# Kernel optimization log

Hardware: AMD Instinct MI355X
Metric: run time of the kernel (lower is better)

Reference implementation:

```python
import jax, jax.numpy as jnp
import numpy as np

B, E, T, N = 1024, 512, 8, 256


def setup_inputs() -> dict:
    key = jax.random.key(0)
    k1, k2, k3, k4 = jax.random.split(key, 4)
    weights = jax.random.uniform(k1, (T,), dtype=jnp.float32)  # one scalar per bond type
    bond_src = jax.random.randint(k2, (B, E), 0, N - 1, dtype=jnp.int32)  # raw i, offset +1 later
    bond_dst = jax.random.randint(k3, (B, E), 0, N - 1, dtype=jnp.int32)
    bond_type = jax.random.randint(k4, (B, E), 0, T, dtype=jnp.int32)
    return {"weights": weights, "bond_src": bond_src, "bond_dst": bond_dst,
            "bond_type": bond_type, "num_nodes": N}


def reference(weights, bond_src, bond_dst, bond_type, num_nodes):
    # Gather per-bond weight, then symmetric scatter into dense [B, N, N] adjacency.
    batch, n_edges = bond_src.shape
    w = weights[bond_type]                                  # [B, E] gather
    bidx = jnp.broadcast_to(jnp.arange(batch)[:, None], (batch, n_edges))
    src = bond_src + 1                                      # +1 node offset as in torch code
    dst = bond_dst + 1
    bond_matrix = jnp.zeros((batch, num_nodes, num_nodes), dtype=weights.dtype)
    bond_matrix = bond_matrix.at[bidx, src, dst].set(w)
    bond_matrix = bond_matrix.at[bidx, dst, src].set(w)
    return bond_matrix
```

## Files before the change

kernel.cpp:

```cpp
#include <hip/hip_runtime.h>


#define NB_E 512
#define NB_N 256
#define CH_ROWS 64
#define CH_WORDS (CH_ROWS * NB_N / 2)

typedef float v4f __attribute__((ext_vector_type(4)));

__device__ __forceinline__ void lds_max_u16(unsigned int* tab, int cell, unsigned int v16)
{
    unsigned int* w = tab + (cell >> 1);
    const int sh = (cell & 1) * 16;
    unsigned int old = *w;
    while (true) {
        const unsigned int cur = (old >> sh) & 0xFFFFu;
        if (cur >= v16) break;
        const unsigned int nw = (old & ~(0xFFFFu << sh)) | (v16 << sh);
        const unsigned int seen = atomicCAS(w, old, nw);
        if (seen == old) break;
        old = seen;
    }
}

__global__ __launch_bounds__(256) void BondWeight_41738492182540_kernel(
    const float* __restrict__ weights,
    const int*   __restrict__ bsrc,
    const int*   __restrict__ bdst,
    const int*   __restrict__ btyp,
    float*       __restrict__ out)
{
    __shared__ unsigned int seqtab[CH_WORDS];
    __shared__ float s_wt[8];

    const int b = blockIdx.x;
    const int t = threadIdx.x;

    if (t < 8) s_wt[t] = weights[t];

    const int ebase = b * NB_E;
    int row[4], col[4];
    unsigned int pk[4];
    #pragma unroll
    for (int i = 0; i < 2; ++i) {
        const int e  = t + 256 * i;
        const int s1 = bsrc[ebase + e] + 1;
        const int d1 = bdst[ebase + e] + 1;
        const unsigned int ty = (unsigned int)btyp[ebase + e] & 7u;
        row[2*i]   = s1; col[2*i]   = d1; pk[2*i]   = ((unsigned int)(e + 1) << 3) | ty;
        row[2*i+1] = d1; col[2*i+1] = s1; pk[2*i+1] = ((unsigned int)(NB_E + e + 1) << 3) | ty;
    }

    {
        uint4* tab4 = (uint4*)seqtab;
        #pragma unroll
        for (int k = 0; k < CH_WORDS / 4 / 256; ++k)
            tab4[t + 256 * k] = make_uint4(0u, 0u, 0u, 0u);
    }
    __syncthreads();

    float4* __restrict__ out4 = ((float4*)out) + (size_t)b * (NB_N * NB_N / 4);
    uint2*  __restrict__ tab2 = (uint2*)seqtab;

    for (int r0 = 0; r0 < NB_N; r0 += CH_ROWS) {
        #pragma unroll
        for (int i = 0; i < 4; ++i) {
            const int r = row[i] - r0;
            if (0 <= r && r < CH_ROWS)
                lds_max_u16(seqtab, r * NB_N + col[i], pk[i]);
        }
        __syncthreads();

        #pragma unroll
        for (int k = 0; k < (CH_ROWS * NB_N / 4) / 256; ++k) {
            const int i4 = t + 256 * k;
            const uint2 ab = tab2[i4];
            tab2[i4] = make_uint2(0u, 0u);
            v4f v;
            unsigned int p;
            p = ab.x & 0xFFFFu; v.x = p ? s_wt[p & 7u] : 0.0f;
            p = ab.x >> 16;     v.y = p ? s_wt[p & 7u] : 0.0f;
            p = ab.y & 0xFFFFu; v.z = p ? s_wt[p & 7u] : 0.0f;
            p = ab.y >> 16;     v.w = p ? s_wt[p & 7u] : 0.0f;
            *(v4f*)&out4[r0 * (NB_N / 4) + i4] = v;
        }
        __syncthreads();
    }
}

extern "C" void kernel_launch(void* const* d_in, const int* in_sizes, int n_in,
                              void* d_out, int out_size, void* d_ws, size_t ws_size,
                              hipStream_t stream) {
    const float* weights = (const float*)d_in[0];
    const int*   bsrc    = (const int*)d_in[1];
    const int*   bdst    = (const int*)d_in[2];
    const int*   btyp    = (const int*)d_in[3];
    float*       out     = (float*)d_out;

    const int nb = in_sizes[1] / NB_E;

    BondWeight_41738492182540_kernel<<<nb, 256, 0, stream>>>(
        weights, bsrc, bdst, btyp, out);
}
```

Baseline: 268.8 us.

## Split into bulk zero-fill kernel and sparse per-chunk scatter kernel

Replaces the per-batch block that builds each dense row chunk in LDS and writes it out with two kernels. A grid-stride kernel zero-fills the whole output, and a second kernel splits each batch into four row-chunk blocks that resolve last-writer conflicts in LDS and store only the surviving nonzero entries. This aims to turn the dense, serialized LDS-to-global writeout into a pure streaming memset plus sparse stores, and to raise parallelism. In exchange it adds a second launch, redundant input reads per chunk, and uncoalesced scattered stores.

```diff
diff --git a/kernel.cpp b/kernel.cpp
--- a/kernel.cpp
+++ b/kernel.cpp
@@ -7,6 +7,16 @@
 #define CH_WORDS (CH_ROWS * NB_N / 2)
 
 typedef float v4f __attribute__((ext_vector_type(4)));
+
+__global__ __launch_bounds__(256) void BondWeight_zero_kernel(
+    float* __restrict__ out, int total4)
+{
+    v4f* __restrict__ o = (v4f*)out;
+    const v4f z = {0.f, 0.f, 0.f, 0.f};
+    const int stride = gridDim.x * 256;
+    for (int k = blockIdx.x * 256 + threadIdx.x; k < total4; k += stride)
+        o[k] = z;
+}
 
 __device__ __forceinline__ void lds_max_u16(unsigned int* tab, int cell, unsigned int v16)
 {
@@ -23,7 +33,7 @@
     }
 }
 
-__global__ __launch_bounds__(256) void BondWeight_41738492182540_kernel(
+__global__ __launch_bounds__(256) void BondWeight_scatter_kernel(
     const float* __restrict__ weights,
     const int*   __restrict__ bsrc,
     const int*   __restrict__ bdst,
@@ -33,10 +43,18 @@
     __shared__ unsigned int seqtab[CH_WORDS];
     __shared__ float s_wt[8];
 
-    const int b = blockIdx.x;
-    const int t = threadIdx.x;
+    const int b  = blockIdx.x >> 2;
+    const int r0 = (blockIdx.x & 3) * CH_ROWS;
+    const int t  = threadIdx.x;
 
     if (t < 8) s_wt[t] = weights[t];
+
+    {
+        uint4* tab4 = (uint4*)seqtab;
+        #pragma unroll
+        for (int k = 0; k < CH_WORDS / 4 / 256; ++k)
+            tab4[t + 256 * k] = make_uint4(0u, 0u, 0u, 0u);
+    }
 
     const int ebase = b * NB_E;
     int row[4], col[4];
@@ -50,41 +68,27 @@
         row[2*i]   = s1; col[2*i]   = d1; pk[2*i]   = ((unsigned int)(e + 1) << 3) | ty;
         row[2*i+1] = d1; col[2*i+1] = s1; pk[2*i+1] = ((unsigned int)(NB_E + e + 1) << 3) | ty;
     }
+    __syncthreads();
 
-    {
-        uint4* tab4 = (uint4*)seqtab;
-        #pragma unroll
-        for (int k = 0; k < CH_WORDS / 4 / 256; ++k)
-            tab4[t + 256 * k] = make_uint4(0u, 0u, 0u, 0u);
+    #pragma unroll
+    for (int i = 0; i < 4; ++i) {
+        const int r = row[i] - r0;
+        if (0 <= r && r < CH_ROWS)
+            lds_max_u16(seqtab, r * NB_N + col[i], pk[i]);
     }
     __syncthreads();
 
-    float4* __restrict__ out4 = ((float4*)out) + (size_t)b * (NB_N * NB_N / 4);
-    uint2*  __restrict__ tab2 = (uint2*)seqtab;
-
-    for (int r0 = 0; r0 < NB_N; r0 += CH_ROWS) {
-        #pragma unroll
-        for (int i = 0; i < 4; ++i) {
-            const int r = row[i] - r0;
-            if (0 <= r && r < CH_ROWS)
-                lds_max_u16(seqtab, r * NB_N + col[i], pk[i]);
+    float* __restrict__ ob = out + (size_t)b * (NB_N * NB_N);
+    #pragma unroll
+    for (int i = 0; i < 4; ++i) {
+        const int r = row[i] - r0;
+        if (0 <= r && r < CH_ROWS) {
+            const int cell = r * NB_N + col[i];
+            const unsigned int cur =
+                (seqtab[cell >> 1] >> ((cell & 1) * 16)) & 0xFFFFu;
+            if (cur == pk[i])
+                ob[(size_t)(r0 + r) * NB_N + col[i]] = s_wt[pk[i] & 7u];
         }
-        __syncthreads();
-
-        #pragma unroll
-        for (int k = 0; k < (CH_ROWS * NB_N / 4) / 256; ++k) {
-            const int i4 = t + 256 * k;
-            const uint2 ab = tab2[i4];
-            tab2[i4] = make_uint2(0u, 0u);
-            v4f v;
-            unsigned int p;
-            p = ab.x & 0xFFFFu; v.x = p ? s_wt[p & 7u] : 0.0f;
-            p = ab.x >> 16;     v.y = p ? s_wt[p & 7u] : 0.0f;
-            p = ab.y & 0xFFFFu; v.z = p ? s_wt[p & 7u] : 0.0f;
-            p = ab.y >> 16;     v.w = p ? s_wt[p & 7u] : 0.0f;
-            *(v4f*)&out4[r0 * (NB_N / 4) + i4] = v;
-        }
-        __syncthreads();
     }
 }
 
@@ -98,7 +102,10 @@
     float*       out     = (float*)d_out;
 
     const int nb = in_sizes[1] / NB_E;
+    const int total4 = nb * (NB_N * NB_N / 4);
 
-    BondWeight_41738492182540_kernel<<<nb, 256, 0, stream>>>(
+    BondWeight_zero_kernel<<<2048, 256, 0, stream>>>(out, total4);
+
+    BondWeight_scatter_kernel<<<nb * 4, 256, 0, stream>>>(
         weights, bsrc, bdst, btyp, out);
 }
```

Result: slower. 315.3 us (+17.3%).
